# Optimization experiments

Hardware: AMD Instinct MI355X
Metric: run time of the kernel (lower is better)

Reference implementation:

```python
import jax, jax.numpy as jnp
import numpy as np
from functools import partial

B, T, IN, H, NC, L = 2048, 512, 64, 64, 4, 2


def _lstm_layer(x, w_ih, w_hh, b_ih, b_hh):
    """Single PyTorch-convention LSTM layer. x: [B,T,Din]; gates ordered i,f,g,o.
    Returns full hidden sequence [B,T,H]."""
    Bx = x.shape[0]
    Hh = w_hh.shape[1]
    # precompute input contribution for all timesteps: [T,B,4H]
    xg = jnp.einsum('bti,gi->tbg', x, w_ih) + (b_ih + b_hh)

    def step(carry, xg_t):
        h, c = carry
        gates = xg_t + h @ w_hh.T  # [B,4H]
        i, f, g, o = jnp.split(gates, 4, axis=-1)
        i = jax.nn.sigmoid(i)
        f = jax.nn.sigmoid(f)
        g = jnp.tanh(g)
        o = jax.nn.sigmoid(o)
        c = f * c + i * g
        h = o * jnp.tanh(c)
        return (h, c), h

    h0 = jnp.zeros((Bx, Hh), dtype=x.dtype)
    c0 = jnp.zeros((Bx, Hh), dtype=x.dtype)
    (_, _), hs = jax.lax.scan(step, (h0, c0), xg)  # hs: [T,B,H]
    return jnp.swapaxes(hs, 0, 1)  # [B,T,H]


def setup_inputs() -> dict:
    key = jax.random.key(0)
    ks = jax.random.split(key, 16)
    s_in = 1.0 / np.sqrt(H)
    inp = {"x": jax.random.normal(ks[0], (B, T, IN), dtype=jnp.float32)}
    dims = [IN, H]
    for l in range(L):
        inp[f"w_ih{l}"] = jax.random.uniform(ks[1 + 4 * l], (4 * H, dims[l]), jnp.float32, -s_in, s_in)
        inp[f"w_hh{l}"] = jax.random.uniform(ks[2 + 4 * l], (4 * H, H), jnp.float32, -s_in, s_in)
        inp[f"b_ih{l}"] = jax.random.uniform(ks[3 + 4 * l], (4 * H,), jnp.float32, -s_in, s_in)
        inp[f"b_hh{l}"] = jax.random.uniform(ks[4 + 4 * l], (4 * H,), jnp.float32, -s_in, s_in)
    inp["fc_w"] = jax.random.uniform(ks[9], (NC, H), jnp.float32, -s_in, s_in)
    inp["fc_b"] = jax.random.uniform(ks[10], (NC,), jnp.float32, -s_in, s_in)
    return inp


def reference(x, w_ih0, w_hh0, b_ih0, b_hh0, w_ih1, w_hh1, b_ih1, b_hh1, fc_w, fc_b):
    # layer 0
    h1 = _lstm_layer(x, w_ih0, w_hh0, b_ih0, b_hh0)   # [B,T,H]
    # inter-layer dropout: identity at inference
    h2 = _lstm_layer(h1, w_ih1, w_hh1, b_ih1, b_hh1)  # [B,T,H]
    last = h2[:, -1, :]                                # [B,H]; dropout = identity (eval)
    return last @ fc_w.T + fc_b                        # [B,NC]
```

## Files before the change

kernel.cpp:

```cpp
#include <hip/hip_runtime.h>
#include <stdint.h>


#define T_SEQ  512
#define NB     4
#define PSTR   136
#define PANEL  (16 * PSTR)
#define PSTR2  72
#define PANEL2 (16 * PSTR2)

typedef __attribute__((ext_vector_type(8))) _Float16 half8;
typedef __attribute__((ext_vector_type(4))) float    float4v;

__device__ __forceinline__ float sigm(float x) {
    return __builtin_amdgcn_rcpf(1.0f + __builtin_amdgcn_exp2f(-1.44269504088896f * x));
}
__device__ __forceinline__ float tanh_f(float x) {
    float e = __builtin_amdgcn_exp2f(-2.88539008177793f * x);
    return __builtin_fmaf(2.0f, __builtin_amdgcn_rcpf(1.0f + e), -1.0f);
}

__global__ __launch_bounds__(256, 2) void lstm2_kernel(
    const float* __restrict__ x,
    const float* __restrict__ wih0, const float* __restrict__ whh0,
    const float* __restrict__ bih0, const float* __restrict__ bhh0,
    const float* __restrict__ wih1, const float* __restrict__ whh1,
    const float* __restrict__ bih1, const float* __restrict__ bhh1,
    const float* __restrict__ fcw,  const float* __restrict__ fcb,
    float* __restrict__ out)
{
    __shared__ __align__(16) unsigned short panel0[2][PANEL];
    __shared__ __align__(16) unsigned short panel1[2][PANEL2];
    __shared__ float h2buf[NB * 64];
    __shared__ float fcw_s[256];
    __shared__ float fcb_s[4];

    const int tid  = threadIdx.x;
    const int lane = tid & 63;
    const int wave = tid >> 6;
    const int mrow = lane & 15;
    const int kg   = lane >> 4;
    const int b0   = blockIdx.x * NB;

    fcw_s[tid & 255] = fcw[tid & 255];
    if (tid < 4) fcb_s[tid] = fcb[tid];
    for (int i = tid; i < 2 * PANEL; i += 256)  panel0[0][i] = 0;
    for (int i = tid; i < 2 * PANEL2; i += 256) panel1[0][i] = 0;

    const int hcol = wave * 16 + mrow;

    float bias0[4], bias1[4];
    #pragma unroll
    for (int g = 0; g < 4; ++g) {
        const int idx = g * 64 + hcol;
        bias0[g] = bih0[idx] + bhh0[idx];
        bias1[g] = bih1[idx] + bhh1[idx];
    }

    half8 wf[2][4][4];
    #pragma unroll
    for (int l = 0; l < 2; ++l) {
        const float* wihp = l ? wih1 : wih0;
        const float* whhp = l ? whh1 : whh0;
        #pragma unroll
        for (int g = 0; g < 4; ++g) {
            const int n = (g * 4 + wave) * 16 + mrow;
            #pragma unroll
            for (int kt = 0; kt < 4; ++kt) {
                const int k0 = kt * 32 + kg * 8;
                const float* src = (k0 < 64) ? (wihp + n * 64 + k0)
                                             : (whhp + n * 64 + (k0 - 64));
                half8 hv8;
                #pragma unroll
                for (int j = 0; j < 8; ++j) hv8[j] = (_Float16)src[j];
                wf[l][g][kt] = hv8;
            }
        }
    }

    __syncthreads();
    const int sxof = 4 * wave * PSTR + lane;
    {
        float xv = x[((size_t)(b0 + wave) * T_SEQ + 0) * 64 + lane];
        panel0[0][sxof] = __builtin_bit_cast(unsigned short, (_Float16)xv);
    }
    __syncthreads();

    const int fragoff  = mrow * PSTR  + kg * 8;
    const int fragoff2 = mrow * PSTR2 + kg * 8;
    const int h0off = 4 * kg * PSTR  + 64 + hcol;
    const int h1off = 4 * kg * PSTR2 + hcol;

    float xcur = x[((size_t)(b0 + wave) * T_SEQ + 1) * 64 + lane];
    const float* xp = x + ((size_t)(b0 + wave) * T_SEQ + 2) * 64 + lane;

    float c0 = 0.f, c1 = 0.f;
    const float4v z4 = {0.f, 0.f, 0.f, 0.f};

    for (int s = 0; s <= T_SEQ; ++s) {
        const int p     = s & 1;
        const int poff  = p * PANEL;
        const int poff2 = p * PANEL2;
        const int qoff  = poff  ^ PANEL;
        const int qoff2 = poff2 ^ PANEL2;

        const bool ld = (s + 2) < T_SEQ;
        float xnext = 0.f;
        if (ld) xnext = *xp;

        const unsigned short* P0 = &panel0[0][0] + poff  + fragoff;
        const unsigned short* P1 = &panel1[0][0] + poff2 + fragoff2;
        half8 af0 = *(const half8*)(P0);
        half8 af1 = *(const half8*)(P0 + 32);
        half8 af2 = *(const half8*)(P0 + 64);
        half8 af3 = *(const half8*)(P0 + 96);
        half8 ag2 = *(const half8*)(P1);
        half8 ag3 = *(const half8*)(P1 + 32);

        float4v a0[4], a1[4];
        #pragma unroll
        for (int g = 0; g < 4; ++g) {
            a0[g] = __builtin_amdgcn_mfma_f32_16x16x32_f16(af0, wf[0][g][0], z4, 0, 0, 0);
            a1[g] = __builtin_amdgcn_mfma_f32_16x16x32_f16(af2, wf[1][g][0], z4, 0, 0, 0);
        }
        #pragma unroll
        for (int g = 0; g < 4; ++g) {
            a0[g] = __builtin_amdgcn_mfma_f32_16x16x32_f16(af1, wf[0][g][1], a0[g], 0, 0, 0);
            a1[g] = __builtin_amdgcn_mfma_f32_16x16x32_f16(af3, wf[1][g][1], a1[g], 0, 0, 0);
        }
        #pragma unroll
        for (int g = 0; g < 4; ++g) {
            a0[g] = __builtin_amdgcn_mfma_f32_16x16x32_f16(af2, wf[0][g][2], a0[g], 0, 0, 0);
            a1[g] = __builtin_amdgcn_mfma_f32_16x16x32_f16(ag2, wf[1][g][2], a1[g], 0, 0, 0);
        }
        #pragma unroll
        for (int g = 0; g < 4; ++g) {
            a0[g] = __builtin_amdgcn_mfma_f32_16x16x32_f16(af3, wf[0][g][3], a0[g], 0, 0, 0);
            a1[g] = __builtin_amdgcn_mfma_f32_16x16x32_f16(ag3, wf[1][g][3], a1[g], 0, 0, 0);
        }

        if (s < T_SEQ) {
            float g0 = a0[0][0] + bias0[0];
            float g1 = a0[1][0] + bias0[1];
            float g2 = a0[2][0] + bias0[2];
            float g3 = a0[3][0] + bias0[3];
            float ig = sigm(g0), fg = sigm(g1);
            float gt = tanh_f(g2), og = sigm(g3);
            c0 = fg * c0 + ig * gt;
            float hv = og * tanh_f(c0);
            panel0[0][qoff + h0off] = __builtin_bit_cast(unsigned short, (_Float16)hv);
        }
        if (s > 0) {
            float g0 = a1[0][0] + bias1[0];
            float g1 = a1[1][0] + bias1[1];
            float g2 = a1[2][0] + bias1[2];
            float g3 = a1[3][0] + bias1[3];
            float ig = sigm(g0), fg = sigm(g1);
            float gt = tanh_f(g2), og = sigm(g3);
            c1 = fg * c1 + ig * gt;
            float hv = og * tanh_f(c1);
            panel1[0][qoff2 + h1off] = __builtin_bit_cast(unsigned short, (_Float16)hv);
            if (s == T_SEQ) h2buf[(kg << 6) + hcol] = hv;
        }
        if (s + 1 < T_SEQ) {
            panel0[0][qoff + sxof] = __builtin_bit_cast(unsigned short, (_Float16)xcur);
        }
        xcur = xnext;
        if (ld) xp += 64;
        __syncthreads();
    }

    if (tid < 16) {
        const int bb = tid >> 2, nc = tid & 3;
        float s = fcb_s[nc];
        #pragma unroll 8
        for (int h = 0; h < 64; ++h) s += h2buf[bb * 64 + h] * fcw_s[nc * 64 + h];
        out[(size_t)(b0 + bb) * 4 + nc] = s;
    }
}

extern "C" void kernel_launch(void* const* d_in, const int* in_sizes, int n_in,
                              void* d_out, int out_size, void* d_ws, size_t ws_size,
                              hipStream_t stream) {
    const float* x    = (const float*)d_in[0];
    const float* wih0 = (const float*)d_in[1];
    const float* whh0 = (const float*)d_in[2];
    const float* bih0 = (const float*)d_in[3];
    const float* bhh0 = (const float*)d_in[4];
    const float* wih1 = (const float*)d_in[5];
    const float* whh1 = (const float*)d_in[6];
    const float* bih1 = (const float*)d_in[7];
    const float* bhh1 = (const float*)d_in[8];
    const float* fcw  = (const float*)d_in[9];
    const float* fcb  = (const float*)d_in[10];
    float* out = (float*)d_out;
    (void)d_ws; (void)ws_size; (void)in_sizes; (void)n_in; (void)out_size;

    lstm2_kernel<<<dim3(2048 / NB), dim3(256), 0, stream>>>(
        x, wih0, whh0, bih0, bhh0, wih1, whh1, bih1, bhh1, fcw, fcb, out);
}
```

Before: 694.7 us.

## Split LSTM layers across separate wave sets in 512-thread blocks

Doubles the block to 512 threads so waves 0-3 compute layer 0 and waves 4-7 compute layer 1, instead of each wave running both layers' MFMA chains. This halves the per-wave serial MFMA and activation work per timestep and halves the weight register footprint, which allows higher occupancy (launch bounds 512,4). It also raises MFMA priority with s_setprio and replaces __syncthreads with a raw lgkmcnt wait plus s_barrier. The cost is a barrier across twice as many waves every step, and some loads and writes become conditional on the wave set. The raw barrier does not wait on the global x loads, which relies on the xnext register being used only in the next step.

```diff
diff --git a/kernel.cpp b/kernel.cpp
--- a/kernel.cpp
+++ b/kernel.cpp
@@ -12,6 +12,8 @@
 typedef __attribute__((ext_vector_type(8))) _Float16 half8;
 typedef __attribute__((ext_vector_type(4))) float    float4v;
 
+#define LBAR() asm volatile("s_waitcnt lgkmcnt(0)\n\ts_barrier" ::: "memory")
+
 __device__ __forceinline__ float sigm(float x) {
     return __builtin_amdgcn_rcpf(1.0f + __builtin_amdgcn_exp2f(-1.44269504088896f * x));
 }
@@ -20,7 +22,7 @@
     return __builtin_fmaf(2.0f, __builtin_amdgcn_rcpf(1.0f + e), -1.0f);
 }
 
-__global__ __launch_bounds__(256, 2) void lstm2_kernel(
+__global__ __launch_bounds__(512, 4) void lstm2_kernel(
     const float* __restrict__ x,
     const float* __restrict__ wih0, const float* __restrict__ whh0,
     const float* __restrict__ bih0, const float* __restrict__ bhh0,
@@ -40,61 +42,66 @@
     const int wave = tid >> 6;
     const int mrow = lane & 15;
     const int kg   = lane >> 4;
+    const int lset = wave >> 2;
+    const int ws   = wave & 3;
     const int b0   = blockIdx.x * NB;
 
-    fcw_s[tid & 255] = fcw[tid & 255];
+    for (int i = tid; i < 256; i += 512) fcw_s[i] = fcw[i];
     if (tid < 4) fcb_s[tid] = fcb[tid];
-    for (int i = tid; i < 2 * PANEL; i += 256)  panel0[0][i] = 0;
-    for (int i = tid; i < 2 * PANEL2; i += 256) panel1[0][i] = 0;
+    for (int i = tid; i < 2 * PANEL; i += 512)  panel0[0][i] = 0;
+    for (int i = tid; i < 2 * PANEL2; i += 512) panel1[0][i] = 0;
 
-    const int hcol = wave * 16 + mrow;
+    const float* wih  = lset ? wih1 : wih0;
+    const float* whh  = lset ? whh1 : whh0;
+    const float* bihp = lset ? bih1 : bih0;
+    const float* bhhp = lset ? bhh1 : bhh0;
 
-    float bias0[4], bias1[4];
+    const int hcol = ws * 16 + mrow;
+
+    float biasg[4];
     #pragma unroll
     for (int g = 0; g < 4; ++g) {
         const int idx = g * 64 + hcol;
-        bias0[g] = bih0[idx] + bhh0[idx];
-        bias1[g] = bih1[idx] + bhh1[idx];
+        biasg[g] = bihp[idx] + bhhp[idx];
     }
 
-    half8 wf[2][4][4];
+    half8 wf[4][4];
     #pragma unroll
-    for (int l = 0; l < 2; ++l) {
-        const float* wihp = l ? wih1 : wih0;
-        const float* whhp = l ? whh1 : whh0;
+    for (int g = 0; g < 4; ++g) {
+        const int n = (g * 4 + ws) * 16 + mrow;
         #pragma unroll
-        for (int g = 0; g < 4; ++g) {
-            const int n = (g * 4 + wave) * 16 + mrow;
+        for (int kt = 0; kt < 4; ++kt) {
+            const int k0 = kt * 32 + kg * 8;
+            const float* src = (k0 < 64) ? (wih + n * 64 + k0)
+                                         : (whh + n * 64 + (k0 - 64));
+            half8 hv8;
             #pragma unroll
-            for (int kt = 0; kt < 4; ++kt) {
-                const int k0 = kt * 32 + kg * 8;
-                const float* src = (k0 < 64) ? (wihp + n * 64 + k0)
-                                             : (whhp + n * 64 + (k0 - 64));
-                half8 hv8;
-                #pragma unroll
-                for (int j = 0; j < 8; ++j) hv8[j] = (_Float16)src[j];
-                wf[l][g][kt] = hv8;
-            }
+            for (int j = 0; j < 8; ++j) hv8[j] = (_Float16)src[j];
+            wf[g][kt] = hv8;
         }
     }
 
     __syncthreads();
-    const int sxof = 4 * wave * PSTR + lane;
-    {
-        float xv = x[((size_t)(b0 + wave) * T_SEQ + 0) * 64 + lane];
+    const int sxof = 4 * ws * PSTR + lane;
+    if (lset == 1) {
+        float xv = x[((size_t)(b0 + ws) * T_SEQ + 0) * 64 + lane];
         panel0[0][sxof] = __builtin_bit_cast(unsigned short, (_Float16)xv);
     }
     __syncthreads();
 
-    const int fragoff  = mrow * PSTR  + kg * 8;
-    const int fragoff2 = mrow * PSTR2 + kg * 8;
+    const int fragoff0 = mrow * PSTR  + kg * 8;
+    const int fragoff1 = mrow * PSTR2 + kg * 8;
+    const unsigned short* rdA = &panel0[0][0] + fragoff0 + (lset ? 64 : 0);
+    const unsigned short* rdB = lset ? (&panel1[0][0] + fragoff1)
+                                     : (&panel0[0][0] + fragoff0 + 64);
     const int h0off = 4 * kg * PSTR  + 64 + hcol;
     const int h1off = 4 * kg * PSTR2 + hcol;
 
-    float xcur = x[((size_t)(b0 + wave) * T_SEQ + 1) * 64 + lane];
-    const float* xp = x + ((size_t)(b0 + wave) * T_SEQ + 2) * 64 + lane;
+    float xcur = 0.f;
+    const float* xp = x + ((size_t)(b0 + ws) * T_SEQ + 2) * 64 + lane;
+    if (lset == 1) xcur = x[((size_t)(b0 + ws) * T_SEQ + 1) * 64 + lane];
 
-    float c0 = 0.f, c1 = 0.f;
+    float c = 0.f;
     const float4v z4 = {0.f, 0.f, 0.f, 0.f};
 
     for (int s = 0; s <= T_SEQ; ++s) {
@@ -104,70 +111,57 @@
         const int qoff  = poff  ^ PANEL;
         const int qoff2 = poff2 ^ PANEL2;
 
-        const bool ld = (s + 2) < T_SEQ;
+        const bool ld = (lset == 1) && ((s + 2) < T_SEQ);
         float xnext = 0.f;
         if (ld) xnext = *xp;
 
-        const unsigned short* P0 = &panel0[0][0] + poff  + fragoff;
-        const unsigned short* P1 = &panel1[0][0] + poff2 + fragoff2;
-        half8 af0 = *(const half8*)(P0);
-        half8 af1 = *(const half8*)(P0 + 32);
-        half8 af2 = *(const half8*)(P0 + 64);
-        half8 af3 = *(const half8*)(P0 + 96);
-        half8 ag2 = *(const half8*)(P1);
-        half8 ag3 = *(const half8*)(P1 + 32);
+        const unsigned short* pA = rdA + poff;
+        const unsigned short* pB = rdB + (lset ? poff2 : poff);
+        half8 af0 = *(const half8*)(pA);
+        half8 af1 = *(const half8*)(pA + 32);
+        half8 af2 = *(const half8*)(pB);
+        half8 af3 = *(const half8*)(pB + 32);
 
-        float4v a0[4], a1[4];
+        __builtin_amdgcn_s_setprio(1);
+        float4v acc[4];
         #pragma unroll
-        for (int g = 0; g < 4; ++g) {
-            a0[g] = __builtin_amdgcn_mfma_f32_16x16x32_f16(af0, wf[0][g][0], z4, 0, 0, 0);
-            a1[g] = __builtin_amdgcn_mfma_f32_16x16x32_f16(af2, wf[1][g][0], z4, 0, 0, 0);
-        }
+        for (int g = 0; g < 4; ++g)
+            acc[g] = __builtin_amdgcn_mfma_f32_16x16x32_f16(af0, wf[g][0], z4, 0, 0, 0);
         #pragma unroll
-        for (int g = 0; g < 4; ++g) {
-            a0[g] = __builtin_amdgcn_mfma_f32_16x16x32_f16(af1, wf[0][g][1], a0[g], 0, 0, 0);
-            a1[g] = __builtin_amdgcn_mfma_f32_16x16x32_f16(af3, wf[1][g][1], a1[g], 0, 0, 0);
-        }
+        for (int g = 0; g < 4; ++g)
+            acc[g] = __builtin_amdgcn_mfma_f32_16x16x32_f16(af1, wf[g][1], acc[g], 0, 0, 0);
         #pragma unroll
-        for (int g = 0; g < 4; ++g) {
-            a0[g] = __builtin_amdgcn_mfma_f32_16x16x32_f16(af2, wf[0][g][2], a0[g], 0, 0, 0);
-            a1[g] = __builtin_amdgcn_mfma_f32_16x16x32_f16(ag2, wf[1][g][2], a1[g], 0, 0, 0);
-        }
+        for (int g = 0; g < 4; ++g)
+            acc[g] = __builtin_amdgcn_mfma_f32_16x16x32_f16(af2, wf[g][2], acc[g], 0, 0, 0);
         #pragma unroll
-        for (int g = 0; g < 4; ++g) {
-            a0[g] = __builtin_amdgcn_mfma_f32_16x16x32_f16(af3, wf[0][g][3], a0[g], 0, 0, 0);
-            a1[g] = __builtin_amdgcn_mfma_f32_16x16x32_f16(ag3, wf[1][g][3], a1[g], 0, 0, 0);
-        }
+        for (int g = 0; g < 4; ++g)
+            acc[g] = __builtin_amdgcn_mfma_f32_16x16x32_f16(af3, wf[g][3], acc[g], 0, 0, 0);
+        __builtin_amdgcn_s_setprio(0);
 
-        if (s < T_SEQ) {
-            float g0 = a0[0][0] + bias0[0];
-            float g1 = a0[1][0] + bias0[1];
-            float g2 = a0[2][0] + bias0[2];
-            float g3 = a0[3][0] + bias0[3];
+        const bool active = lset ? (s > 0) : (s < T_SEQ);
+        if (active) {
+            float g0 = acc[0][0] + biasg[0];
+            float g1 = acc[1][0] + biasg[1];
+            float g2 = acc[2][0] + biasg[2];
+            float g3 = acc[3][0] + biasg[3];
             float ig = sigm(g0), fg = sigm(g1);
             float gt = tanh_f(g2), og = sigm(g3);
-            c0 = fg * c0 + ig * gt;
-            float hv = og * tanh_f(c0);
-            panel0[0][qoff + h0off] = __builtin_bit_cast(unsigned short, (_Float16)hv);
+            c = fg * c + ig * gt;
+            float hv = og * tanh_f(c);
+            unsigned short hbits = __builtin_bit_cast(unsigned short, (_Float16)hv);
+            if (lset == 0) {
+                panel0[0][qoff + h0off] = hbits;
+            } else {
+                panel1[0][qoff2 + h1off] = hbits;
+                if (s == T_SEQ) h2buf[(kg << 6) + hcol] = hv;
+            }
         }
-        if (s > 0) {
-            float g0 = a1[0][0] + bias1[0];
-            float g1 = a1[1][0] + bias1[1];
-            float g2 = a1[2][0] + bias1[2];
-            float g3 = a1[3][0] + bias1[3];
-            float ig = sigm(g0), fg = sigm(g1);
-            float gt = tanh_f(g2), og = sigm(g3);
-            c1 = fg * c1 + ig * gt;
-            float hv = og * tanh_f(c1);
-            panel1[0][qoff2 + h1off] = __builtin_bit_cast(unsigned short, (_Float16)hv);
-            if (s == T_SEQ) h2buf[(kg << 6) + hcol] = hv;
-        }
-        if (s + 1 < T_SEQ) {
+        if (lset == 1 && (s + 1) < T_SEQ) {
             panel0[0][qoff + sxof] = __builtin_bit_cast(unsigned short, (_Float16)xcur);
         }
         xcur = xnext;
         if (ld) xp += 64;
-        __syncthreads();
+        LBAR();
     }
 
     if (tid < 16) {
@@ -196,6 +190,6 @@
     float* out = (float*)d_out;
     (void)d_ws; (void)ws_size; (void)in_sizes; (void)n_in; (void)out_size;
 
-    lstm2_kernel<<<dim3(2048 / NB), dim3(256), 0, stream>>>(
+    lstm2_kernel<<<dim3(2048 / NB), dim3(512), 0, stream>>>(
         x, wih0, whh0, bih0, bhh0, wih1, whh1, bih1, bhh1, fcw, fcb, out);
 }
```

Result: no change. 699.4 us (+0.7%).
